# Kernel optimization log

Hardware: AMD Instinct MI355X
Metric: run time of the kernel (lower is better)

## Reference

```python
import jax, jax.numpy as jnp
import numpy as np

NUM_LAYERS = 4
D_MODEL = 1024
N_HEAD = 8
HEAD_DIM = D_MODEL // N_HEAD
FFN_DIM = 4096
B, L = 8, 512
LN_EPS = 1e-5


def rel_pos_embed(seq_len, dim, init_size=1200, padding_idx=0):
    # RelativeSinusoidalPositionalEmbedding.get_embedding(init_size+1, dim, 0)
    num = init_size + 1  # 1201
    half = dim // 2
    inv = np.exp(np.arange(half, dtype=np.float64) * -(np.log(10000.0) / (half - 1)))
    pos = np.arange(-num // 2, num // 2, dtype=np.float64)[:, None] * inv[None, :]
    emb = np.concatenate([np.sin(pos), np.cos(pos)], axis=1)  # [num, dim]
    emb[padding_idx] = 0.0
    origin_shift = num // 2 + 1  # 601
    idx = np.arange(-seq_len, seq_len) + origin_shift  # [2L]
    return jnp.asarray(emb[idx], dtype=jnp.float32)  # [2L, dim]


def _shift(BD):
    # [b,h,L,2L] -> [b,h,L,L], selecting relative offsets k-q
    b, h, l, _ = BD.shape
    BD = jnp.concatenate([BD, jnp.zeros((b, h, l, 1), BD.dtype)], axis=-1)
    BD = BD.reshape(b, h, -1, l)[:, :, :-1].reshape(b, h, l, 2 * l)
    return BD[:, :, :, l:]


def _transpose_shift(E):
    # [b,h,L,2L] -> [b,h,L,L]
    b, h, l, _ = E.shape
    E = jnp.concatenate([E, jnp.zeros((b, h, l, 1), E.dtype)], axis=-1)
    E = E.reshape(b, h, 2 * l + 1, l)
    E = E[:, :, 2 * jnp.arange(l) + 1, :]  # [b,h,L,L]
    return jnp.swapaxes(E, -1, -2)


def layer_norm(x, g, b):
    mu = x.mean(-1, keepdims=True)
    var = ((x - mu) ** 2).mean(-1, keepdims=True)
    return (x - mu) / jnp.sqrt(var + LN_EPS) * g + b


def rel_attn(x, mask, qkv_w, r_r, r_w, pos):
    bsz, l, d = x.shape
    qkv = x @ qkv_w  # [b,L,3D]
    q, k, v = jnp.split(qkv, 3, axis=-1)
    to_heads = lambda t: t.reshape(bsz, l, N_HEAD, HEAD_DIM).transpose(0, 2, 1, 3)
    q, k, v = to_heads(q), to_heads(k), to_heads(v)  # [b,h,L,hd]
    rw_q = q + r_r[:, None]  # (original adds r_r_bias here)
    AC = jnp.einsum('bnqd,bnkd->bnqk', rw_q, k)
    D_ = jnp.einsum('nd,ld->nl', r_w, pos)[None, :, None]   # [1,h,1,2L]
    B_ = jnp.einsum('bnqd,ld->bnql', q, pos)                # [b,h,L,2L]
    E_ = jnp.einsum('bnqd,ld->bnql', k, pos)
    BDE = _shift(B_ + D_) + _transpose_shift(E_)
    attn = AC + BDE  # scale == 1 (scale=False)
    attn = jnp.where(mask[:, None, None, :] == 0, -jnp.inf, attn)
    attn = jax.nn.softmax(attn, axis=-1)
    out = jnp.einsum('bnqk,bnkd->bnqd', attn, v)
    return out.transpose(0, 2, 1, 3).reshape(bsz, l, d)


def setup_inputs() -> dict:
    key = jax.random.key(0)
    ks = jax.random.split(key, 12)
    Ln = NUM_LAYERS
    s = 0.02
    return {
        'x': jax.random.normal(ks[0], (B, L, D_MODEL), jnp.float32),
        'mask': jnp.ones((B, L), jnp.int32),
        'qkv_w': jax.random.normal(ks[1], (Ln, D_MODEL, 3 * D_MODEL), jnp.float32) * s,
        'r_r_bias': jax.random.normal(ks[2], (Ln, N_HEAD, HEAD_DIM), jnp.float32) * s,
        'r_w_bias': jax.random.normal(ks[3], (Ln, N_HEAD, HEAD_DIM), jnp.float32) * s,
        'ln1_g': jnp.ones((Ln, D_MODEL), jnp.float32),
        'ln1_b': jnp.zeros((Ln, D_MODEL), jnp.float32),
        'ln2_g': jnp.ones((Ln, D_MODEL), jnp.float32),
        'ln2_b': jnp.zeros((Ln, D_MODEL), jnp.float32),
        'w1': jax.random.normal(ks[4], (Ln, D_MODEL, FFN_DIM), jnp.float32) * s,
        'b1': jnp.zeros((Ln, FFN_DIM), jnp.float32),
        'w2': jax.random.normal(ks[5], (Ln, FFN_DIM, D_MODEL), jnp.float32) * s,
        'b2': jnp.zeros((Ln, D_MODEL), jnp.float32),
    }


def reference(x, mask, qkv_w, r_r_bias, r_w_bias, ln1_g, ln1_b, ln2_g, ln2_b, w1, b1, w2, b2):
    pos = rel_pos_embed(x.shape[1], HEAD_DIM)  # [2L, hd], buffer (detached)
    for i in range(NUM_LAYERS):  # after_norm=True (post-LN)
        a = rel_attn(x, mask, qkv_w[i], r_r_bias[i], r_w_bias[i], pos)
        x = layer_norm(x + a, ln1_g[i], ln1_b[i])
        h = jax.nn.relu(x @ w1[i] + b1[i]) @ w2[i] + b2[i]
        x = layer_norm(x + h, ln2_g[i], ln2_b[i])
    return x
```

## Files before the change

### kernel.cpp

```cpp
#include <hip/hip_runtime.h>

#define SEQ 512
#define DM 1024
#define NH 8
#define HD 128
#define FFN 4096
#define NL 4
#define NB 8

typedef __attribute__((ext_vector_type(8))) _Float16 half8v;
typedef __attribute__((ext_vector_type(8))) unsigned short ushort8v;
typedef __attribute__((ext_vector_type(4))) float float4v;

__device__ __forceinline__ unsigned short f2h(float f) {
  _Float16 h = (_Float16)f;
  return *(unsigned short*)&h;
}
__device__ __forceinline__ float h2f(unsigned short u) {
  _Float16 h = *(_Float16*)&u;
  return (float)h;
}

__global__ void sc_kernel(float* __restrict__ sc) {
  int idx = blockIdx.x * blockDim.x + threadIdx.x;
  int q = idx >> 6, c = idx & 63;
  if (q >= SEQ) return;
  double a = exp(-(double)c * (9.210340371976184 / 63.0));
  double p = (double)q * a;
  sc[q * 128 + c] = (float)sin(p);
  sc[q * 128 + 64 + c] = (float)cos(p);
}

__global__ void cvt_copy(const float* __restrict__ in, float* __restrict__ xout,
                         unsigned short* __restrict__ xh, int n4) {
  int i = blockIdx.x * blockDim.x + threadIdx.x;
  if (i >= n4) return;
  float4 v = ((const float4*)in)[i];
  ((float4*)xout)[i] = v;
  ushort4 u;
  u.x = f2h(v.x); u.y = f2h(v.y); u.z = f2h(v.z); u.w = f2h(v.w);
  ((ushort4*)xh)[i] = u;
}

__global__ __launch_bounds__(256) void transpose_cvt(
    const float* __restrict__ in, unsigned short* __restrict__ out, int K, int N) {
  __shared__ float t[32][33];
  int n0 = blockIdx.x * 32, k0 = blockIdx.y * 32;
  int c = threadIdx.x & 31, r = threadIdx.x >> 5;
#pragma unroll
  for (int i = 0; i < 32; i += 8)
    t[r + i][c] = in[(long long)(k0 + r + i) * N + n0 + c];
  __syncthreads();
#pragma unroll
  for (int i = 0; i < 32; i += 8)
    out[(long long)(n0 + r + i) * K + k0 + c] = f2h(t[c][r + i]);
}

template<int R>
__device__ __forceinline__ void stage_tile(
    const unsigned short* __restrict__ g, long long ld, int k0,
    unsigned short* lds, int tid) {
#pragma unroll
  for (int i = 0; i < R / 32; i++) {
    int p = i * 256 + tid;
    int row = p >> 3, cs = p & 7;
    int c = cs ^ (row & 7);
    const unsigned short* src = g + (long long)row * ld + k0 + c * 8;
    __builtin_amdgcn_global_load_lds(
        (const __attribute__((address_space(1))) void*)src,
        (__attribute__((address_space(3))) void*)(lds + p * 8),
        16, 0, 0);
  }
}

template<int BIAS, int RELU, int OUTH, int NF, int DBUF>
__global__ __launch_bounds__(256) void gemm_mfma(
    const unsigned short* __restrict__ A, int lda,
    const unsigned short* __restrict__ Bt, int ldb,
    const float* __restrict__ bias,
    void* __restrict__ Cv, int ldc,
    int K) {
  const int BN = 32 * NF;
  __shared__ __align__(16) unsigned short Asm[DBUF + 1][128 * 64];
  __shared__ __align__(16) unsigned short Bsm[DBUF + 1][BN * 64];
  const int tid = threadIdx.x, lane = tid & 63, wave = tid >> 6;
  const int wr = wave >> 1, wc = wave & 1;
  int nwg = gridDim.x * gridDim.y;
  int lin = blockIdx.y * gridDim.x + blockIdx.x;
  int swz = (lin & 7) * (nwg >> 3) + (lin >> 3);
  int bx = swz % gridDim.x, by = swz / gridDim.x;
  const unsigned short* Ag = A + (long long)by * 128 * lda;
  const unsigned short* Bg = Bt + (long long)bx * BN * ldb;
  const int l15 = lane & 15, l4 = lane >> 4;
  float4v acc[4][NF] = {};
  if (DBUF) {
    stage_tile<128>(Ag, lda, 0, Asm[0], tid);
    stage_tile<BN>(Bg, ldb, 0, Bsm[0], tid);
  }
  int cur = 0;
  for (int k0 = 0; k0 < K; k0 += 64) {
    if (DBUF) {
      __syncthreads();
      if (k0 + 64 < K) {
        stage_tile<128>(Ag, lda, k0 + 64, Asm[cur ^ 1], tid);
        stage_tile<BN>(Bg, ldb, k0 + 64, Bsm[cur ^ 1], tid);
      }
    } else {
      __syncthreads();
      stage_tile<128>(Ag, lda, k0, Asm[0], tid);
      stage_tile<BN>(Bg, ldb, k0, Bsm[0], tid);
      __syncthreads();
    }
#pragma unroll
    for (int kk = 0; kk < 2; kk++) {
      half8v af[4], bf[NF];
#pragma unroll
      for (int m = 0; m < 4; m++) {
        int row = wr * 64 + m * 16 + l15;
        int cs = (kk * 4 + l4) ^ (row & 7);
        af[m] = *(const half8v*)&Asm[cur][row * 64 + cs * 8];
      }
#pragma unroll
      for (int n = 0; n < NF; n++) {
        int row = wc * 16 * NF + n * 16 + l15;
        int cs = (kk * 4 + l4) ^ (row & 7);
        bf[n] = *(const half8v*)&Bsm[cur][row * 64 + cs * 8];
      }
#pragma unroll
      for (int m = 0; m < 4; m++)
#pragma unroll
        for (int n = 0; n < NF; n++)
          acc[m][n] = __builtin_amdgcn_mfma_f32_16x16x32_f16(af[m], bf[n], acc[m][n], 0, 0, 0);
    }
    if (DBUF) cur ^= 1;
  }
#pragma unroll
  for (int n = 0; n < NF; n++) {
    int ccol = bx * BN + wc * 16 * NF + n * 16 + l15;
    float bv = BIAS ? bias[ccol] : 0.f;
#pragma unroll
    for (int m = 0; m < 4; m++) {
      int crow0 = by * 128 + wr * 64 + m * 16 + l4 * 4;
#pragma unroll
      for (int j = 0; j < 4; j++) {
        float v = acc[m][n][j] + bv;
        if (RELU) v = fmaxf(v, 0.f);
        long long off = (long long)(crow0 + j) * ldc + ccol;
        if (OUTH) ((unsigned short*)Cv)[off] = f2h(v);
        else      ((float*)Cv)[off] = v;
      }
    }
  }
}

template<int OUTH, int ZSH, int NF>
__global__ __launch_bounds__(256) void gemm_mfma_b(
    const unsigned short* __restrict__ A, int lda, long long sAz,
    const unsigned short* __restrict__ Bt, int ldb, long long sBz,
    void* __restrict__ Cv, int ldc, long long sCb, long long sCh,
    int K) {
  const int BN = 32 * NF;
  __shared__ __align__(16) unsigned short Asm[2][128 * 64];
  __shared__ __align__(16) unsigned short Bsm[2][BN * 64];
  const int tid = threadIdx.x, lane = tid & 63, wave = tid >> 6;
  const int wr = wave >> 1, wc = wave & 1;
  const int gx = gridDim.x, gy = gridDim.y;
  int nwg = gx * gy * gridDim.z;
  int lin = (blockIdx.z * gy + blockIdx.y) * gx + blockIdx.x;
  int swz = (lin & 7) * (nwg >> 3) + (lin >> 3);
  int bx = swz % gx;
  int t2 = swz / gx;
  int by = t2 % gy;
  int z  = t2 / gy;
  const int zb = z >> ZSH, zh = z & ((1 << ZSH) - 1);
  const unsigned short* Ag = A + (long long)z * sAz + (long long)by * 128 * lda;
  const unsigned short* Bg = Bt + (long long)z * sBz + (long long)bx * BN * ldb;
  const int l15 = lane & 15, l4 = lane >> 4;
  float4v acc[4][NF] = {};
  stage_tile<128>(Ag, lda, 0, Asm[0], tid);
  stage_tile<BN>(Bg, ldb, 0, Bsm[0], tid);
  int cur = 0;
  for (int k0 = 0; k0 < K; k0 += 64) {
    __syncthreads();
    if (k0 + 64 < K) {
      stage_tile<128>(Ag, lda, k0 + 64, Asm[cur ^ 1], tid);
      stage_tile<BN>(Bg, ldb, k0 + 64, Bsm[cur ^ 1], tid);
    }
#pragma unroll
    for (int kk = 0; kk < 2; kk++) {
      half8v af[4], bf[NF];
#pragma unroll
      for (int m = 0; m < 4; m++) {
        int row = wr * 64 + m * 16 + l15;
        int cs = (kk * 4 + l4) ^ (row & 7);
        af[m] = *(const half8v*)&Asm[cur][row * 64 + cs * 8];
      }
#pragma unroll
      for (int n = 0; n < NF; n++) {
        int row = wc * 16 * NF + n * 16 + l15;
        int cs = (kk * 4 + l4) ^ (row & 7);
        bf[n] = *(const half8v*)&Bsm[cur][row * 64 + cs * 8];
      }
#pragma unroll
      for (int m = 0; m < 4; m++)
#pragma unroll
        for (int n = 0; n < NF; n++)
          acc[m][n] = __builtin_amdgcn_mfma_f32_16x16x32_f16(af[m], bf[n], acc[m][n], 0, 0, 0);
    }
    cur ^= 1;
  }
  long long cbase = (long long)zb * sCb + (long long)zh * sCh;
#pragma unroll
  for (int n = 0; n < NF; n++) {
    int ccol = bx * BN + wc * 16 * NF + n * 16 + l15;
#pragma unroll
    for (int m = 0; m < 4; m++) {
      int crow0 = by * 128 + wr * 64 + m * 16 + l4 * 4;
#pragma unroll
      for (int j = 0; j < 4; j++) {
        float v = acc[m][n][j];
        long long off = cbase + (long long)(crow0 + j) * ldc + ccol;
        if (OUTH) ((unsigned short*)Cv)[off] = f2h(v);
        else      ((float*)Cv)[off] = v;
      }
    }
  }
}

__global__ __launch_bounds__(256) void build_aug(
    const unsigned short* __restrict__ qkv_h,
    const float* __restrict__ rr, const float* __restrict__ rw,
    const float* __restrict__ sc,
    unsigned short* __restrict__ Ahat, unsigned short* __restrict__ Bhat)
{
  const int z = blockIdx.y, b = z >> 3, h = z & 7;
  const int r = threadIdx.x >> 7, lane = threadIdx.x & 127;
  const int q = blockIdx.x * 2 + r;
  __shared__ float Qf[2][128], Kf[2][128], SC[2][128];
  const unsigned short* row = qkv_h + ((long long)(b * SEQ + q)) * 3072 + h * HD;
  float qv = h2f(row[lane]);
  float kv = h2f(row[DM + lane]);
  Qf[r][lane] = qv + rw[h * HD + lane];
  Kf[r][lane] = kv;
  SC[r][lane] = sc[q * 128 + lane];
  __syncthreads();
  unsigned short* Arow = Ahat + ((long long)z * SEQ + q) * 384;
  unsigned short* Brow = Bhat + ((long long)z * SEQ + q) * 384;
  Arow[lane] = f2h(qv + rr[h * HD + lane]);
  Brow[lane] = f2h(kv);
  if (lane < 64) {
    float S = SC[r][lane], C = SC[r][64 + lane];
    Arow[128 + lane] = f2h(Qf[r][lane] * C + Qf[r][64 + lane] * S);
    Arow[256 + lane] = f2h(S);
    Brow[128 + lane] = f2h(S);
    Brow[256 + lane] = f2h(Kf[r][lane] * C + Kf[r][64 + lane] * S);
  } else {
    int c = lane - 64;
    float S = SC[r][c], C = SC[r][lane];
    Arow[192 + c] = f2h(Qf[r][lane] * C - Qf[r][c] * S);
    Arow[320 + c] = f2h(C);
    Brow[192 + c] = f2h(C);
    Brow[320 + c] = f2h(Kf[r][lane] * C - Kf[r][c] * S);
  }
}

__global__ __launch_bounds__(256) void transpose_v(
    const unsigned short* __restrict__ qkv_h, unsigned short* __restrict__ Vt)
{
  __shared__ unsigned short t[32][33];
  const int z = blockIdx.z, b = z >> 3, h = z & 7;
  const int d0 = blockIdx.x * 32, j0 = blockIdx.y * 32;
  const int c = threadIdx.x & 31, r = threadIdx.x >> 5;
#pragma unroll
  for (int i = 0; i < 32; i += 8)
    t[r + i][c] = qkv_h[((long long)(b * SEQ + j0 + r + i)) * 3072 + 2 * DM + h * HD + d0 + c];
  __syncthreads();
#pragma unroll
  for (int i = 0; i < 32; i += 8)
    Vt[(long long)z * HD * SEQ + (long long)(d0 + r + i) * SEQ + j0 + c] = t[c][r + i];
}

__global__ __launch_bounds__(256) void softmax_mask_h(
    unsigned short* __restrict__ scores16, const int* __restrict__ mask)
{
  const int z = blockIdx.y, b = z >> 3;
  const int wid = threadIdx.x >> 6, lane = threadIdx.x & 63;
  const int q = blockIdx.x * 4 + wid;
  unsigned short* row = scores16 + ((long long)z * SEQ + q) * SEQ;
  ushort8v u = ((ushort8v*)row)[lane];
  const int4* mp = (const int4*)(mask + (size_t)b * SEQ);
  int4 m0 = mp[lane * 2], m1 = mp[lane * 2 + 1];
  const int mk[8] = {m0.x, m0.y, m0.z, m0.w, m1.x, m1.y, m1.z, m1.w};
  float v[8];
  float mx = -1e30f;
#pragma unroll
  for (int i = 0; i < 8; i++) {
    v[i] = mk[i] ? h2f(u[i]) : -1e30f;
    mx = fmaxf(mx, v[i]);
  }
#pragma unroll
  for (int o = 32; o; o >>= 1) mx = fmaxf(mx, __shfl_xor(mx, o));
  float e[8], s = 0.f;
#pragma unroll
  for (int i = 0; i < 8; i++) { e[i] = __expf(v[i] - mx); s += e[i]; }
#pragma unroll
  for (int o = 32; o; o >>= 1) s += __shfl_xor(s, o);
  float inv = 1.f / s;
#pragma unroll
  for (int i = 0; i < 8; i++) u[i] = f2h(e[i] * inv);
  ((ushort8v*)row)[lane] = u;
}

__global__ __launch_bounds__(256) void add_ln_cvt(
    float* __restrict__ x, const float* __restrict__ a,
    const float* __restrict__ g, const float* __restrict__ bt,
    unsigned short* __restrict__ xh)
{
  const int row = blockIdx.x, tid = threadIdx.x;
  float4* xp = (float4*)(x + (size_t)row * DM);
  const float4* ap = (const float4*)(a + (size_t)row * DM);
  float4 xv = xp[tid], av = ap[tid];
  float4 s = make_float4(xv.x + av.x, xv.y + av.y, xv.z + av.z, xv.w + av.w);
  __shared__ float red[4];
  float sum = s.x + s.y + s.z + s.w;
  for (int o = 32; o; o >>= 1) sum += __shfl_down(sum, o);
  if ((tid & 63) == 0) red[tid >> 6] = sum;
  __syncthreads();
  float mu = (red[0] + red[1] + red[2] + red[3]) * (1.f / DM);
  float dx = s.x - mu, dy = s.y - mu, dz = s.z - mu, dw = s.w - mu;
  float sq = dx * dx + dy * dy + dz * dz + dw * dw;
  for (int o = 32; o; o >>= 1) sq += __shfl_down(sq, o);
  __syncthreads();
  if ((tid & 63) == 0) red[tid >> 6] = sq;
  __syncthreads();
  float var = (red[0] + red[1] + red[2] + red[3]) * (1.f / DM);
  float rstd = rsqrtf(var + 1e-5f);
  const float4 gv = ((const float4*)g)[tid];
  const float4 bv = ((const float4*)bt)[tid];
  float4 o4 = make_float4(dx * rstd * gv.x + bv.x, dy * rstd * gv.y + bv.y,
                          dz * rstd * gv.z + bv.z, dw * rstd * gv.w + bv.w);
  xp[tid] = o4;
  ushort4 u;
  u.x = f2h(o4.x); u.y = f2h(o4.y); u.z = f2h(o4.z); u.w = f2h(o4.w);
  ((ushort4*)(xh + (size_t)row * DM))[tid] = u;
}

__global__ __launch_bounds__(256) void add_ln_cvt2(
    float* __restrict__ x, const float* __restrict__ p0, const float* __restrict__ p1,
    const float* __restrict__ bias,
    const float* __restrict__ g, const float* __restrict__ bt,
    unsigned short* __restrict__ xh)
{
  const int row = blockIdx.x, tid = threadIdx.x;
  float4* xp = (float4*)(x + (size_t)row * DM);
  const float4 a0 = ((const float4*)(p0 + (size_t)row * DM))[tid];
  const float4 a1 = ((const float4*)(p1 + (size_t)row * DM))[tid];
  const float4 bb = ((const float4*)bias)[tid];
  float4 xv = xp[tid];
  float4 s = make_float4(xv.x + a0.x + a1.x + bb.x, xv.y + a0.y + a1.y + bb.y,
                         xv.z + a0.z + a1.z + bb.z, xv.w + a0.w + a1.w + bb.w);
  __shared__ float red[4];
  float sum = s.x + s.y + s.z + s.w;
  for (int o = 32; o; o >>= 1) sum += __shfl_down(sum, o);
  if ((tid & 63) == 0) red[tid >> 6] = sum;
  __syncthreads();
  float mu = (red[0] + red[1] + red[2] + red[3]) * (1.f / DM);
  float dx = s.x - mu, dy = s.y - mu, dz = s.z - mu, dw = s.w - mu;
  float sq = dx * dx + dy * dy + dz * dz + dw * dw;
  for (int o = 32; o; o >>= 1) sq += __shfl_down(sq, o);
  __syncthreads();
  if ((tid & 63) == 0) red[tid >> 6] = sq;
  __syncthreads();
  float var = (red[0] + red[1] + red[2] + red[3]) * (1.f / DM);
  float rstd = rsqrtf(var + 1e-5f);
  const float4 gv = ((const float4*)g)[tid];
  const float4 bv = ((const float4*)bt)[tid];
  float4 o4 = make_float4(dx * rstd * gv.x + bv.x, dy * rstd * gv.y + bv.y,
                          dz * rstd * gv.z + bv.z, dw * rstd * gv.w + bv.w);
  xp[tid] = o4;
  ushort4 u;
  u.x = f2h(o4.x); u.y = f2h(o4.y); u.z = f2h(o4.z); u.w = f2h(o4.w);
  ((ushort4*)(xh + (size_t)row * DM))[tid] = u;
}

extern "C" void kernel_launch(void* const* d_in, const int* in_sizes, int n_in,
                              void* d_out, int out_size, void* d_ws, size_t ws_size,
                              hipStream_t stream)
{
  const float* x_in = (const float*)d_in[0];
  const int*   mask = (const int*)d_in[1];
  const float* qkv_w = (const float*)d_in[2];
  const float* r_r  = (const float*)d_in[3];
  const float* r_w  = (const float*)d_in[4];
  const float* ln1g = (const float*)d_in[5];
  const float* ln1b = (const float*)d_in[6];
  const float* ln2g = (const float*)d_in[7];
  const float* ln2b = (const float*)d_in[8];
  const float* w1   = (const float*)d_in[9];
  const float* b1   = (const float*)d_in[10];
  const float* w2   = (const float*)d_in[11];
  const float* b2   = (const float*)d_in[12];
  float* x = (float*)d_out;
  char* ws = (char*)d_ws;

  const int ROWS = NB * SEQ;

  const size_t sc_off   = 0;
  const size_t xh_off   = 0x40000;
  const size_t wt_off   = xh_off + (size_t)ROWS * DM * 2;
  const size_t f_off    = wt_off + (size_t)FFN * DM * 2;
  const size_t qkvh_off = f_off + 2 * (size_t)ROWS * DM * 4;
  const size_t e_off    = qkvh_off + (size_t)ROWS * 3 * DM * 2;

  const size_t ffn_need = (size_t)ROWS * FFN * 2;
  int nb = 8;
  while (nb > 1) {
    size_t ab = (size_t)nb * 8 * SEQ * 384 * 2;
    size_t vt = (size_t)nb * 8 * HD * SEQ * 2;
    size_t scb = (size_t)nb * 8 * SEQ * SEQ * 2;
    size_t att_need = 2 * ab + vt + scb;
    size_t need = e_off + (att_need > ffn_need ? att_need : ffn_need);
    if (need <= ws_size) break;
    nb >>= 1;
  }
  const size_t ab_bytes = (size_t)nb * 8 * SEQ * 384 * 2;
  const size_t vt_bytes = (size_t)nb * 8 * HD * SEQ * 2;

  float* sc     = (float*)(ws + sc_off);
  unsigned short* xh = (unsigned short*)(ws + xh_off);
  unsigned short* wt = (unsigned short*)(ws + wt_off);
  float* aout   = (float*)(ws + f_off);
  float* fbuf   = (float*)(ws + f_off);
  unsigned short* qkvh = (unsigned short*)(ws + qkvh_off);
  unsigned short* Ahat = (unsigned short*)(ws + e_off);
  unsigned short* Bhat = (unsigned short*)(ws + e_off + ab_bytes);
  unsigned short* Vt   = (unsigned short*)(ws + e_off + 2 * ab_bytes);
  unsigned short* scores16 = (unsigned short*)(ws + e_off + 2 * ab_bytes + vt_bytes);
  unsigned short* hb = (unsigned short*)(ws + e_off);

  sc_kernel<<<dim3(SEQ * 64 / 256), 256, 0, stream>>>(sc);
  cvt_copy<<<dim3(ROWS * DM / 4 / 256), 256, 0, stream>>>(x_in, x, xh, ROWS * DM / 4);

  for (int L = 0; L < NL; L++) {
    transpose_cvt<<<dim3(3 * DM / 32, DM / 32), 256, 0, stream>>>(
        qkv_w + (size_t)L * DM * 3 * DM, wt, DM, 3 * DM);
    gemm_mfma<0,0,1,4,0><<<dim3(3 * DM / 128, ROWS / 128), 256, 0, stream>>>(
        xh, DM, wt, DM, nullptr, qkvh, 3 * DM, DM);

    for (int b0 = 0; b0 < NB; b0 += nb) {
      const unsigned short* qkvh_b = qkvh + (size_t)b0 * SEQ * 3072;
      build_aug<<<dim3(SEQ / 2, nb * 8), 256, 0, stream>>>(
          qkvh_b, r_r + (size_t)L * NH * HD, r_w + (size_t)L * NH * HD, sc, Ahat, Bhat);
      transpose_v<<<dim3(HD / 32, SEQ / 32, nb * 8), 256, 0, stream>>>(qkvh_b, Vt);
      gemm_mfma_b<1,0,2><<<dim3(SEQ / 64, SEQ / 128, nb * 8), 256, 0, stream>>>(
          Ahat, 384, (long long)SEQ * 384,
          Bhat, 384, (long long)SEQ * 384,
          scores16, SEQ, (long long)SEQ * SEQ, 0, 384);
      softmax_mask_h<<<dim3(SEQ / 4, nb * 8), 256, 0, stream>>>(scores16, mask + (size_t)b0 * SEQ);
      gemm_mfma_b<0,3,2><<<dim3(HD / 64, SEQ / 128, nb * 8), 256, 0, stream>>>(
          scores16, SEQ, (long long)SEQ * SEQ,
          Vt, SEQ, (long long)HD * SEQ,
          aout + (size_t)b0 * SEQ * DM, DM, (long long)SEQ * DM, HD, SEQ);
    }
    add_ln_cvt<<<dim3(ROWS), 256, 0, stream>>>(x, aout, ln1g + (size_t)L * DM, ln1b + (size_t)L * DM, xh);

    transpose_cvt<<<dim3(FFN / 32, DM / 32), 256, 0, stream>>>(
        w1 + (size_t)L * DM * FFN, wt, DM, FFN);
    gemm_mfma<1,1,1,4,0><<<dim3(FFN / 128, ROWS / 128), 256, 0, stream>>>(
        xh, DM, wt, DM, b1 + (size_t)L * FFN, hb, FFN, DM);

    transpose_cvt<<<dim3(DM / 32, FFN / 32), 256, 0, stream>>>(
        w2 + (size_t)L * FFN * DM, wt, FFN, DM);
    gemm_mfma_b<0,0,2><<<dim3(DM / 64, ROWS / 128, 2), 256, 0, stream>>>(
        hb, FFN, 2048,
        wt, FFN, 2048,
        fbuf, DM, (long long)ROWS * DM, 0, 2048);

    add_ln_cvt2<<<dim3(ROWS), 256, 0, stream>>>(
        x, fbuf, fbuf + (size_t)ROWS * DM, b2 + (size_t)L * DM,
        ln2g + (size_t)L * DM, ln2b + (size_t)L * DM, xh);
  }
}
```

Before: 1.028 ms.

## Retile batched GEMMs, add single-buffer variant, split-K 4 for FFN2, fp16 attn out

Adds a single-buffer LDS variant of the batched GEMM so 128x128 tiles (NF=4) fit. The score GEMM and the FFN second GEMM now use it, and FFN2 switches from split-K 2 to split-K 4 with a four-partial LayerNorm reduction. The attention output is written as fp16 and read back in the first add+LN, which halves that traffic. The trade-offs are the loss of copy/compute overlap in the single-buffered kernels, extra partial-sum traffic for FFN2, and some precision loss on the attention output.

```diff
diff --git a/kernel.cpp b/kernel.cpp
--- a/kernel.cpp
+++ b/kernel.cpp
@@ -153,15 +153,15 @@
   }
 }
 
-template<int OUTH, int ZSH, int NF>
-__global__ __launch_bounds__(256) void gemm_mfma_b(
+template<int OUTH, int ZSH, int NF, int DBUF>
+__global__ __launch_bounds__(256) void gemm_bat(
     const unsigned short* __restrict__ A, int lda, long long sAz,
     const unsigned short* __restrict__ Bt, int ldb, long long sBz,
     void* __restrict__ Cv, int ldc, long long sCb, long long sCh,
     int K) {
   const int BN = 32 * NF;
-  __shared__ __align__(16) unsigned short Asm[2][128 * 64];
-  __shared__ __align__(16) unsigned short Bsm[2][BN * 64];
+  __shared__ __align__(16) unsigned short Asm[DBUF + 1][128 * 64];
+  __shared__ __align__(16) unsigned short Bsm[DBUF + 1][BN * 64];
   const int tid = threadIdx.x, lane = tid & 63, wave = tid >> 6;
   const int wr = wave >> 1, wc = wave & 1;
   const int gx = gridDim.x, gy = gridDim.y;
@@ -177,14 +177,23 @@
   const unsigned short* Bg = Bt + (long long)z * sBz + (long long)bx * BN * ldb;
   const int l15 = lane & 15, l4 = lane >> 4;
   float4v acc[4][NF] = {};
-  stage_tile<128>(Ag, lda, 0, Asm[0], tid);
-  stage_tile<BN>(Bg, ldb, 0, Bsm[0], tid);
+  if (DBUF) {
+    stage_tile<128>(Ag, lda, 0, Asm[0], tid);
+    stage_tile<BN>(Bg, ldb, 0, Bsm[0], tid);
+  }
   int cur = 0;
   for (int k0 = 0; k0 < K; k0 += 64) {
-    __syncthreads();
-    if (k0 + 64 < K) {
-      stage_tile<128>(Ag, lda, k0 + 64, Asm[cur ^ 1], tid);
-      stage_tile<BN>(Bg, ldb, k0 + 64, Bsm[cur ^ 1], tid);
+    if (DBUF) {
+      __syncthreads();
+      if (k0 + 64 < K) {
+        stage_tile<128>(Ag, lda, k0 + 64, Asm[cur ^ 1], tid);
+        stage_tile<BN>(Bg, ldb, k0 + 64, Bsm[cur ^ 1], tid);
+      }
+    } else {
+      __syncthreads();
+      stage_tile<128>(Ag, lda, k0, Asm[0], tid);
+      stage_tile<BN>(Bg, ldb, k0, Bsm[0], tid);
+      __syncthreads();
     }
 #pragma unroll
     for (int kk = 0; kk < 2; kk++) {
@@ -207,7 +216,7 @@
         for (int n = 0; n < NF; n++)
           acc[m][n] = __builtin_amdgcn_mfma_f32_16x16x32_f16(af[m], bf[n], acc[m][n], 0, 0, 0);
     }
-    cur ^= 1;
+    if (DBUF) cur ^= 1;
   }
   long long cbase = (long long)zb * sCb + (long long)zh * sCh;
 #pragma unroll
@@ -312,15 +321,16 @@
 }
 
 __global__ __launch_bounds__(256) void add_ln_cvt(
-    float* __restrict__ x, const float* __restrict__ a,
+    float* __restrict__ x, const unsigned short* __restrict__ a,
     const float* __restrict__ g, const float* __restrict__ bt,
     unsigned short* __restrict__ xh)
 {
   const int row = blockIdx.x, tid = threadIdx.x;
   float4* xp = (float4*)(x + (size_t)row * DM);
-  const float4* ap = (const float4*)(a + (size_t)row * DM);
-  float4 xv = xp[tid], av = ap[tid];
-  float4 s = make_float4(xv.x + av.x, xv.y + av.y, xv.z + av.z, xv.w + av.w);
+  const ushort4 av = ((const ushort4*)(a + (size_t)row * DM))[tid];
+  float4 xv = xp[tid];
+  float4 s = make_float4(xv.x + h2f(av.x), xv.y + h2f(av.y),
+                         xv.z + h2f(av.z), xv.w + h2f(av.w));
   __shared__ float red[4];
   float sum = s.x + s.y + s.z + s.w;
   for (int o = 32; o; o >>= 1) sum += __shfl_down(sum, o);
@@ -345,20 +355,22 @@
   ((ushort4*)(xh + (size_t)row * DM))[tid] = u;
 }
 
-__global__ __launch_bounds__(256) void add_ln_cvt2(
-    float* __restrict__ x, const float* __restrict__ p0, const float* __restrict__ p1,
+__global__ __launch_bounds__(256) void add_ln_cvt4(
+    float* __restrict__ x, const float* __restrict__ p, long long pstride,
     const float* __restrict__ bias,
     const float* __restrict__ g, const float* __restrict__ bt,
     unsigned short* __restrict__ xh)
 {
   const int row = blockIdx.x, tid = threadIdx.x;
   float4* xp = (float4*)(x + (size_t)row * DM);
-  const float4 a0 = ((const float4*)(p0 + (size_t)row * DM))[tid];
-  const float4 a1 = ((const float4*)(p1 + (size_t)row * DM))[tid];
   const float4 bb = ((const float4*)bias)[tid];
   float4 xv = xp[tid];
-  float4 s = make_float4(xv.x + a0.x + a1.x + bb.x, xv.y + a0.y + a1.y + bb.y,
-                         xv.z + a0.z + a1.z + bb.z, xv.w + a0.w + a1.w + bb.w);
+  float4 s = make_float4(xv.x + bb.x, xv.y + bb.y, xv.z + bb.z, xv.w + bb.w);
+#pragma unroll
+  for (int zz = 0; zz < 4; zz++) {
+    const float4 a = ((const float4*)(p + zz * pstride + (size_t)row * DM))[tid];
+    s.x += a.x; s.y += a.y; s.z += a.z; s.w += a.w;
+  }
   __shared__ float red[4];
   float sum = s.x + s.y + s.z + s.w;
   for (int o = 32; o; o >>= 1) sum += __shfl_down(sum, o);
@@ -408,11 +420,14 @@
   const size_t sc_off   = 0;
   const size_t xh_off   = 0x40000;
   const size_t wt_off   = xh_off + (size_t)ROWS * DM * 2;
-  const size_t f_off    = wt_off + (size_t)FFN * DM * 2;
-  const size_t qkvh_off = f_off + 2 * (size_t)ROWS * DM * 4;
+  const size_t a16_off  = wt_off + (size_t)FFN * DM * 2;
+  const size_t qkvh_off = a16_off + (size_t)ROWS * DM * 2;
   const size_t e_off    = qkvh_off + (size_t)ROWS * 3 * DM * 2;
 
-  const size_t ffn_need = (size_t)ROWS * FFN * 2;
+  const size_t hb_bytes = (size_t)ROWS * FFN * 2;
+  const size_t part_off = e_off + hb_bytes;
+  const size_t ffn_need = hb_bytes + 4 * (size_t)ROWS * DM * 4;
+
   int nb = 8;
   while (nb > 1) {
     size_t ab = (size_t)nb * 8 * SEQ * 384 * 2;
@@ -429,14 +444,14 @@
   float* sc     = (float*)(ws + sc_off);
   unsigned short* xh = (unsigned short*)(ws + xh_off);
   unsigned short* wt = (unsigned short*)(ws + wt_off);
-  float* aout   = (float*)(ws + f_off);
-  float* fbuf   = (float*)(ws + f_off);
+  unsigned short* a16 = (unsigned short*)(ws + a16_off);
   unsigned short* qkvh = (unsigned short*)(ws + qkvh_off);
   unsigned short* Ahat = (unsigned short*)(ws + e_off);
   unsigned short* Bhat = (unsigned short*)(ws + e_off + ab_bytes);
   unsigned short* Vt   = (unsigned short*)(ws + e_off + 2 * ab_bytes);
   unsigned short* scores16 = (unsigned short*)(ws + e_off + 2 * ab_bytes + vt_bytes);
   unsigned short* hb = (unsigned short*)(ws + e_off);
+  float* part = (float*)(ws + part_off);
 
   sc_kernel<<<dim3(SEQ * 64 / 256), 256, 0, stream>>>(sc);
   cvt_copy<<<dim3(ROWS * DM / 4 / 256), 256, 0, stream>>>(x_in, x, xh, ROWS * DM / 4);
@@ -452,17 +467,17 @@
       build_aug<<<dim3(SEQ / 2, nb * 8), 256, 0, stream>>>(
           qkvh_b, r_r + (size_t)L * NH * HD, r_w + (size_t)L * NH * HD, sc, Ahat, Bhat);
       transpose_v<<<dim3(HD / 32, SEQ / 32, nb * 8), 256, 0, stream>>>(qkvh_b, Vt);
-      gemm_mfma_b<1,0,2><<<dim3(SEQ / 64, SEQ / 128, nb * 8), 256, 0, stream>>>(
+      gemm_bat<1,0,4,0><<<dim3(SEQ / 128, SEQ / 128, nb * 8), 256, 0, stream>>>(
           Ahat, 384, (long long)SEQ * 384,
           Bhat, 384, (long long)SEQ * 384,
           scores16, SEQ, (long long)SEQ * SEQ, 0, 384);
       softmax_mask_h<<<dim3(SEQ / 4, nb * 8), 256, 0, stream>>>(scores16, mask + (size_t)b0 * SEQ);
-      gemm_mfma_b<0,3,2><<<dim3(HD / 64, SEQ / 128, nb * 8), 256, 0, stream>>>(
+      gemm_bat<1,3,2,1><<<dim3(HD / 64, SEQ / 128, nb * 8), 256, 0, stream>>>(
           scores16, SEQ, (long long)SEQ * SEQ,
           Vt, SEQ, (long long)HD * SEQ,
-          aout + (size_t)b0 * SEQ * DM, DM, (long long)SEQ * DM, HD, SEQ);
-    }
-    add_ln_cvt<<<dim3(ROWS), 256, 0, stream>>>(x, aout, ln1g + (size_t)L * DM, ln1b + (size_t)L * DM, xh);
+          a16 + (size_t)b0 * SEQ * DM, DM, (long long)SEQ * DM, HD, SEQ);
+    }
+    add_ln_cvt<<<dim3(ROWS), 256, 0, stream>>>(x, a16, ln1g + (size_t)L * DM, ln1b + (size_t)L * DM, xh);
 
     transpose_cvt<<<dim3(FFN / 32, DM / 32), 256, 0, stream>>>(
         w1 + (size_t)L * DM * FFN, wt, DM, FFN);
@@ -471,13 +486,13 @@
 
     transpose_cvt<<<dim3(DM / 32, FFN / 32), 256, 0, stream>>>(
         w2 + (size_t)L * FFN * DM, wt, FFN, DM);
-    gemm_mfma_b<0,0,2><<<dim3(DM / 64, ROWS / 128, 2), 256, 0, stream>>>(
-        hb, FFN, 2048,
-        wt, FFN, 2048,
-        fbuf, DM, (long long)ROWS * DM, 0, 2048);
-
-    add_ln_cvt2<<<dim3(ROWS), 256, 0, stream>>>(
-        x, fbuf, fbuf + (size_t)ROWS * DM, b2 + (size_t)L * DM,
+    gemm_bat<0,0,4,0><<<dim3(DM / 128, ROWS / 128, 4), 256, 0, stream>>>(
+        hb, FFN, 1024,
+        wt, FFN, 1024,
+        part, DM, (long long)ROWS * DM, 0, 1024);
+
+    add_ln_cvt4<<<dim3(ROWS), 256, 0, stream>>>(
+        x, part, (long long)ROWS * DM, b2 + (size_t)L * DM,
         ln2g + (size_t)L * DM, ln2b + (size_t)L * DM, xh);
   }
 }
```

New measurement: 1.018 ms. About the same (-0.9%).
